# Optimization experiments

Hardware: AMD Instinct MI355X
Metric: run time of the kernel (lower is better)

## Reference

```python
import jax, jax.numpy as jnp
import numpy as np

GAMMA = 0.5
SCALE_BASE = 512.0
LN_EPS = 1e-5


def _xpos(x, downscale=False):
    # x: (B, S, Dh); RetNet XPOS rotary embedding (Jamie-Stirling impl)
    S, Dh = x.shape[1], x.shape[2]
    half = Dh // 2
    base_scale = (jnp.arange(0, Dh, 2, dtype=jnp.float32) + 0.4 * Dh) / (1.4 * Dh)  # (half,)
    power = jnp.arange(S, dtype=jnp.float32)[:, None] / SCALE_BASE                   # (S,1)
    scale = base_scale[None, :] ** power                                             # (S,half)
    inv_freq = 1.0 / (10000.0 ** (jnp.arange(half, dtype=jnp.float32) / half))       # (half,)
    sinusoid = jnp.arange(S, dtype=jnp.float32)[:, None] * inv_freq[None, :]         # (S,half)
    sin, cos = jnp.sin(sinusoid), jnp.cos(sinusoid)
    if downscale:
        scale = 1.0 / scale
    # duplicate_interleave: (S,half) -> (S,Dh) repeating each column twice
    sin_s = jnp.repeat(sin * scale, 2, axis=-1)
    cos_s = jnp.repeat(cos * scale, 2, axis=-1)
    x1, x2 = x[..., ::2], x[..., 1::2]
    rot = jnp.stack((-x2, x1), axis=-1).reshape(x.shape)  # rotate_every_two
    return x * cos_s + rot * sin_s


def _decay_mask(S):
    n = jnp.arange(S)
    diff = (n[:, None] - n[None, :]).astype(jnp.float32)
    return jnp.where(n[:, None] >= n[None, :], GAMMA ** diff, 0.0)  # (S,S)


def setup_inputs() -> dict:
    key = jax.random.key(0)
    ks = jax.random.split(key, 10)
    D, d = 768, 192
    hw, b, s = 196, 8, 32
    x = jax.random.normal(ks[0], (hw, b * s, D), dtype=jnp.float32)
    scale_in = 1.0 / np.sqrt(D)
    scale_d = 1.0 / np.sqrt(d)
    return {
        "x": x,
        "W1": jax.random.normal(ks[1], (D, d), dtype=jnp.float32) * scale_in,
        "b1": jnp.zeros((d,), dtype=jnp.float32),
        "W2": jax.random.normal(ks[2], (d, D), dtype=jnp.float32) * scale_d,
        "b2": jnp.zeros((D,), dtype=jnp.float32),
        "ln_g": jnp.ones((d,), dtype=jnp.float32),
        "ln_b": jnp.zeros((d,), dtype=jnp.float32),
        "WQ": jax.random.normal(ks[3], (d, d), dtype=jnp.float32) * scale_d,
        "WK": jax.random.normal(ks[4], (d, d), dtype=jnp.float32) * scale_d,
        "WV": jax.random.normal(ks[5], (d, d), dtype=jnp.float32) * scale_d,
        "batch_dim": 8,
        "seq_dim": 32,
        "hw": 196,
    }


def reference(x, W1, b1, W2, b2, ln_g, ln_b, WQ, WK, WV, batch_dim, seq_dim, hw):
    D = x.shape[-1]
    # (hw, b*s, D) -> (b*hw, s, D)
    xr = x.reshape(hw, batch_dim, seq_dim, D).transpose(1, 0, 2, 3)
    xr = xr.reshape(batch_dim * hw, seq_dim, D)
    x_down = xr @ W1 + b1  # (B, s, d)
    # LayerNorm
    mu = jnp.mean(x_down, axis=-1, keepdims=True)
    var = jnp.mean((x_down - mu) ** 2, axis=-1, keepdims=True)
    h = (x_down - mu) / jnp.sqrt(var + LN_EPS) * ln_g + ln_b
    # SimpleRetention (parallel form)
    Q = _xpos(h @ WQ, downscale=False)
    K = _xpos(h @ WK, downscale=True)
    V = h @ WV
    Dmask = _decay_mask(seq_dim)  # (s,s)
    att = jnp.einsum("bnd,bmd->bnm", Q, K) * Dmask[None]
    ret = att @ V  # (B, s, d)
    out = xr + (ret @ W2 + b2)
    # (b*hw, s, D) -> (hw, b*s, D)
    out = out.reshape(batch_dim, hw, seq_dim, D).transpose(1, 0, 2, 3)
    return out.reshape(hw, batch_dim * seq_dim, D)
```

## Files before the change

kernel.cpp:

```cpp
#include <hip/hip_runtime.h>

typedef __bf16 bf16x8 __attribute__((ext_vector_type(8)));
typedef __bf16 bf16x4 __attribute__((ext_vector_type(4)));
typedef float floatx4 __attribute__((ext_vector_type(4)));

__device__ __forceinline__ __bf16 f2bf(float f) {
  union { float f; unsigned u; } x; x.f = f;
  unsigned r = (x.u + 0x7FFFu + ((x.u >> 16) & 1u)) >> 16;
  union { unsigned short u; __bf16 b; } o; o.u = (unsigned short)r; return o.b;
}
__device__ __forceinline__ float bf2f(__bf16 b) {
  union { unsigned short u; __bf16 b; } i; i.b = b;
  union { unsigned u; float f; } y; y.u = ((unsigned)i.u) << 16; return y.f;
}

#define MFMA16(a, b, c) __builtin_amdgcn_mfma_f32_16x16x32_bf16(a, b, c, 0, 0, 0)

__global__ __launch_bounds__(256) void prep_weights(
    const float* __restrict__ W1, const float* __restrict__ WQ,
    const float* __restrict__ WK, const float* __restrict__ WV,
    const float* __restrict__ W2,
    __bf16* __restrict__ w1f, __bf16* __restrict__ wqf,
    __bf16* __restrict__ wkf, __bf16* __restrict__ wvf,
    __bf16* __restrict__ w2f) {
  int i = blockIdx.x * 256 + threadIdx.x;
  if (i < 147456) {
    int e = i & 7, lane = (i >> 3) & 63, rest = i >> 9;
    int kk32 = rest % 24, nt = rest / 24;
    int n = nt * 16 + (lane & 15), k = kk32 * 32 + (lane >> 4) * 8 + e;
    w1f[i] = f2bf(W1[k * 192 + n]); return;
  }
  i -= 147456;
  if (i < 36864) {
    int e = i & 7, lane = (i >> 3) & 63, rest = i >> 9;
    int kk32 = rest % 6, nt = rest / 6;
    int n = nt * 16 + (lane & 15), k = kk32 * 32 + (lane >> 4) * 8 + e;
    wqf[i] = f2bf(WQ[k * 192 + n]); return;
  }
  i -= 36864;
  if (i < 36864) {
    int e = i & 7, lane = (i >> 3) & 63, rest = i >> 9;
    int kk32 = rest % 6, nt = rest / 6;
    int n = nt * 16 + (lane & 15), k = kk32 * 32 + (lane >> 4) * 8 + e;
    wkf[i] = f2bf(WK[k * 192 + n]); return;
  }
  i -= 36864;
  if (i < 36864) {
    int e = i & 7, lane = (i >> 3) & 63, rest = i >> 9;
    int kk32 = rest % 6, nt = rest / 6;
    int n = nt * 16 + (lane & 15), k = kk32 * 32 + (lane >> 4) * 8 + e;
    wvf[i] = f2bf(WV[k * 192 + n]); return;
  }
  i -= 36864;
  if (i < 147456) {
    int e = i & 7, lane = (i >> 3) & 63, rest = i >> 9;
    int kk32 = rest % 6, nt = rest / 6;
    int n = nt * 16 + (lane & 15), k = kk32 * 32 + (lane >> 4) * 8 + e;
    w2f[i] = f2bf(W2[k * 768 + n]); return;
  }
}

__global__ __launch_bounds__(256) void prep_xf(
    const float* __restrict__ x, __bf16* __restrict__ xf) {
  int j = blockIdx.x * 256 + threadIdx.x;
  int lane = j & 63;
  int rest = j >> 6;
  int kk32 = rest % 24;
  int rest2 = rest / 24;
  size_t row = (size_t)rest2 * 16 + (lane & 15);
  int d = kk32 * 32 + ((lane >> 4) & 3) * 8;
  const float* src = x + row * 768 + d;
  float4 f0 = *(const float4*)(src);
  float4 f1 = *(const float4*)(src + 4);
  bf16x8 a;
  a[0] = f2bf(f0.x); a[1] = f2bf(f0.y); a[2] = f2bf(f0.z); a[3] = f2bf(f0.w);
  a[4] = f2bf(f1.x); a[5] = f2bf(f1.y); a[6] = f2bf(f1.z); a[7] = f2bf(f1.w);
  *(bf16x8*)(xf + (size_t)j * 8) = a;
}

__global__ __launch_bounds__(256) void prep_tables(
    float* __restrict__ cq, float* __restrict__ sq,
    float* __restrict__ ck, float* __restrict__ sk) {
  int i = blockIdx.x * 256 + threadIdx.x;
  if (i >= 32 * 96) return;
  int s = i / 96, f = i % 96;
  float base = (2.f * f + 0.4f * 192.f) / (1.4f * 192.f);
  float scale = powf(base, (float)s / 512.f);
  float invf = powf(10000.f, -(float)f / 96.f);
  float ang = (float)s * invf;
  float sn = sinf(ang), cs = cosf(ang);
  int o = s * 192 + 2 * f;
  cq[o] = cs * scale; cq[o + 1] = cs * scale;
  sq[o] = sn * scale; sq[o + 1] = sn * scale;
  ck[o] = cs / scale; ck[o + 1] = cs / scale;
  sk[o] = sn / scale; sk[o + 1] = sn / scale;
}

#define SW(r, c) ((r) * 192 + ((c) ^ (((r) & 7) << 3)))

template <bool USE_XF>
__global__ __launch_bounds__(256) void retnet_main(
    const float* __restrict__ x, const float* __restrict__ b1,
    const float* __restrict__ b2, const float* __restrict__ ln_g,
    const float* __restrict__ ln_b,
    const __bf16* __restrict__ w1f, const __bf16* __restrict__ wqf,
    const __bf16* __restrict__ wkf, const __bf16* __restrict__ wvf,
    const __bf16* __restrict__ w2f,
    const float* __restrict__ cq, const float* __restrict__ sq,
    const float* __restrict__ ck, const float* __restrict__ sk,
    const __bf16* __restrict__ xf, float* __restrict__ out) {
  __shared__ __align__(16) char smem[51200];
  __bf16* Q = (__bf16*)smem;
  __bf16* Kl = (__bf16*)(smem + 12288);
  __bf16* Vt = (__bf16*)(smem + 24576);
  __bf16* att = (__bf16*)(smem + 36864);
  __bf16* h = (__bf16*)(smem + 38912);

  const int tid = threadIdx.x;
  const int wv = tid >> 6;
  const int lane = tid & 63;
  const int l16 = lane & 15;
  const int quad = lane >> 4;
  const int kof = quad * 8;
  const int p = blockIdx.x;
  const float* xblk = x + (size_t)p * 32 * 768;

  {
    floatx4 acc[2][3] = {};
    if (USE_XF) {
      const __bf16* xfp = xf + (size_t)p * 24576;
#pragma unroll 4
      for (int kk32 = 0; kk32 < 24; ++kk32) {
        bf16x8 a0 = *(const bf16x8*)(xfp + kk32 * 512 + lane * 8);
        bf16x8 a1 = *(const bf16x8*)(xfp + 12288 + kk32 * 512 + lane * 8);
#pragma unroll
        for (int t = 0; t < 3; ++t) {
          bf16x8 bb = *(const bf16x8*)(w1f + (size_t)((wv * 3 + t) * 24 + kk32) * 512 + lane * 8);
          acc[0][t] = MFMA16(a0, bb, acc[0][t]);
          acc[1][t] = MFMA16(a1, bb, acc[1][t]);
        }
      }
    } else {
      const float* arow0 = xblk + l16 * 768;
      const float* arow1 = xblk + (16 + l16) * 768;
#pragma unroll 2
      for (int kk = 0; kk < 768; kk += 32) {
        float4 f0 = *(const float4*)(arow0 + kk + kof);
        float4 f1 = *(const float4*)(arow0 + kk + kof + 4);
        float4 g0 = *(const float4*)(arow1 + kk + kof);
        float4 g1 = *(const float4*)(arow1 + kk + kof + 4);
        bf16x8 a0, a1;
        a0[0] = f2bf(f0.x); a0[1] = f2bf(f0.y); a0[2] = f2bf(f0.z); a0[3] = f2bf(f0.w);
        a0[4] = f2bf(f1.x); a0[5] = f2bf(f1.y); a0[6] = f2bf(f1.z); a0[7] = f2bf(f1.w);
        a1[0] = f2bf(g0.x); a1[1] = f2bf(g0.y); a1[2] = f2bf(g0.z); a1[3] = f2bf(g0.w);
        a1[4] = f2bf(g1.x); a1[5] = f2bf(g1.y); a1[6] = f2bf(g1.z); a1[7] = f2bf(g1.w);
        int kk32 = kk >> 5;
#pragma unroll
        for (int t = 0; t < 3; ++t) {
          bf16x8 bb = *(const bf16x8*)(w1f + (size_t)((wv * 3 + t) * 24 + kk32) * 512 + lane * 8);
          acc[0][t] = MFMA16(a0, bb, acc[0][t]);
          acc[1][t] = MFMA16(a1, bb, acc[1][t]);
        }
      }
    }
#pragma unroll
    for (int m = 0; m < 2; ++m)
#pragma unroll
      for (int t = 0; t < 3; ++t) {
        int col = wv * 48 + t * 16 + l16;
        float bias = b1[col];
#pragma unroll
        for (int r = 0; r < 4; ++r) {
          int row = m * 16 + quad * 4 + r;
          h[SW(row, col)] = f2bf(acc[m][t][r] + bias);
        }
      }
  }
  __syncthreads();

  {
    int r = tid >> 3, g = tid & 7;
    float vals[24]; float s = 0.f, s2 = 0.f;
#pragma unroll
    for (int j = 0; j < 24; ++j) {
      int c = g * 24 + j;
      float v = bf2f(h[SW(r, c)]);
      vals[j] = v; s += v; s2 += v * v;
    }
#pragma unroll
    for (int o = 1; o < 8; o <<= 1) { s += __shfl_xor(s, o); s2 += __shfl_xor(s2, o); }
    float mu = s * (1.f / 192.f);
    float var = s2 * (1.f / 192.f) - mu * mu;
    float rstd = rsqrtf(var + 1e-5f);
#pragma unroll
    for (int j = 0; j < 24; ++j) {
      int c = g * 24 + j;
      h[SW(r, c)] = f2bf((vals[j] - mu) * rstd * ln_g[c] + ln_b[c]);
    }
  }
  __syncthreads();

  auto gemm_h = [&](const __bf16* __restrict__ Wf, floatx4 (&acc)[2][3]) {
#pragma unroll
    for (int kk32 = 0; kk32 < 6; ++kk32) {
      bf16x8 a0 = *(const bf16x8*)(h + SW(l16, kk32 * 32 + kof));
      bf16x8 a1 = *(const bf16x8*)(h + SW(16 + l16, kk32 * 32 + kof));
#pragma unroll
      for (int t = 0; t < 3; ++t) {
        bf16x8 bb = *(const bf16x8*)(Wf + (size_t)((wv * 3 + t) * 6 + kk32) * 512 + lane * 8);
        acc[0][t] = MFMA16(a0, bb, acc[0][t]);
        acc[1][t] = MFMA16(a1, bb, acc[1][t]);
      }
    }
  };
  {
    floatx4 acc[2][3] = {};
    gemm_h(wqf, acc);
#pragma unroll
    for (int m = 0; m < 2; ++m)
#pragma unroll
      for (int t = 0; t < 3; ++t) {
        int col = wv * 48 + t * 16 + l16;
#pragma unroll
        for (int r = 0; r < 4; ++r) {
          int row = m * 16 + quad * 4 + r;
          float v = acc[m][t][r];
          float pr = __shfl_xor(v, 1);
          float o = v * cq[row * 192 + col] + ((lane & 1) ? pr : -pr) * sq[row * 192 + col];
          Q[SW(row, col)] = f2bf(o);
        }
      }
  }
  {
    floatx4 acc[2][3] = {};
    gemm_h(wkf, acc);
#pragma unroll
    for (int m = 0; m < 2; ++m)
#pragma unroll
      for (int t = 0; t < 3; ++t) {
        int col = wv * 48 + t * 16 + l16;
#pragma unroll
        for (int r = 0; r < 4; ++r) {
          int row = m * 16 + quad * 4 + r;
          float v = acc[m][t][r];
          float pr = __shfl_xor(v, 1);
          float o = v * ck[row * 192 + col] + ((lane & 1) ? pr : -pr) * sk[row * 192 + col];
          Kl[SW(row, col)] = f2bf(o);
        }
      }
  }
  {
    floatx4 acc[2][3] = {};
    gemm_h(wvf, acc);
#pragma unroll
    for (int m = 0; m < 2; ++m)
#pragma unroll
      for (int t = 0; t < 3; ++t) {
        int col = wv * 48 + t * 16 + l16;
        bf16x4 pk;
#pragma unroll
        for (int r = 0; r < 4; ++r) pk[r] = f2bf(acc[m][t][r]);
        *(bf16x4*)(Vt + col * 32 + m * 16 + quad * 4) = pk;
      }
  }
  __syncthreads();

  {
    int mt = wv >> 1, nt = wv & 1;
    floatx4 acc = {0.f, 0.f, 0.f, 0.f};
#pragma unroll
    for (int kk = 0; kk < 192; kk += 32) {
      bf16x8 a = *(const bf16x8*)(Q + SW(mt * 16 + l16, kk + kof));
      bf16x8 bb = *(const bf16x8*)(Kl + SW(nt * 16 + l16, kk + kof));
      acc = MFMA16(a, bb, acc);
    }
#pragma unroll
    for (int r = 0; r < 4; ++r) {
      int i = mt * 16 + quad * 4 + r;
      int j = nt * 16 + l16;
      float v = (i >= j) ? acc[r] * exp2f((float)(j - i)) : 0.f;
      att[i * 32 + j] = f2bf(v);
    }
  }
  __syncthreads();

  {
    floatx4 acc[2][3] = {};
    bf16x8 a0 = *(const bf16x8*)(att + l16 * 32 + kof);
    bf16x8 a1 = *(const bf16x8*)(att + (16 + l16) * 32 + kof);
#pragma unroll
    for (int t = 0; t < 3; ++t) {
      bf16x8 bb = *(const bf16x8*)(Vt + (wv * 48 + t * 16 + l16) * 32 + kof);
      acc[0][t] = MFMA16(a0, bb, acc[0][t]);
      acc[1][t] = MFMA16(a1, bb, acc[1][t]);
    }
#pragma unroll
    for (int m = 0; m < 2; ++m)
#pragma unroll
      for (int t = 0; t < 3; ++t) {
        int col = wv * 48 + t * 16 + l16;
#pragma unroll
        for (int r = 0; r < 4; ++r) {
          int row = m * 16 + quad * 4 + r;
          h[SW(row, col)] = f2bf(acc[m][t][r]);
        }
      }
  }
  __syncthreads();

  {
    bf16x8 af[2][6];
#pragma unroll
    for (int k6 = 0; k6 < 6; ++k6) {
      af[0][k6] = *(const bf16x8*)(h + SW(l16, k6 * 32 + kof));
      af[1][k6] = *(const bf16x8*)(h + SW(16 + l16, k6 * 32 + kof));
    }
#pragma unroll
    for (int g = 0; g < 4; ++g) {
      floatx4 acc[2][3] = {};
#pragma unroll
      for (int k6 = 0; k6 < 6; ++k6) {
#pragma unroll
        for (int t = 0; t < 3; ++t) {
          bf16x8 bb = *(const bf16x8*)(w2f + (size_t)((wv * 12 + g * 3 + t) * 6 + k6) * 512 + lane * 8);
          acc[0][t] = MFMA16(af[0][k6], bb, acc[0][t]);
          acc[1][t] = MFMA16(af[1][k6], bb, acc[1][t]);
        }
      }
#pragma unroll
      for (int m = 0; m < 2; ++m)
#pragma unroll
        for (int t = 0; t < 3; ++t) {
          int col = wv * 192 + g * 48 + t * 16 + l16;
          float bias = b2[col];
#pragma unroll
          for (int r = 0; r < 4; ++r) {
            int row = m * 16 + quad * 4 + r;
            size_t gi = (size_t)p * 24576 + row * 768 + col;
            out[gi] = xblk[row * 768 + col] + acc[m][t][r] + bias;
          }
        }
    }
  }
}

extern "C" void kernel_launch(void* const* d_in, const int* in_sizes, int n_in,
                              void* d_out, int out_size, void* d_ws, size_t ws_size,
                              hipStream_t stream) {
  const float* x = (const float*)d_in[0];
  const float* W1 = (const float*)d_in[1];
  const float* b1 = (const float*)d_in[2];
  const float* W2 = (const float*)d_in[3];
  const float* b2 = (const float*)d_in[4];
  const float* lng = (const float*)d_in[5];
  const float* lnb = (const float*)d_in[6];
  const float* WQ = (const float*)d_in[7];
  const float* WK = (const float*)d_in[8];
  const float* WV = (const float*)d_in[9];
  float* out = (float*)d_out;

  char* ws = (char*)d_ws;
  __bf16* w1f = (__bf16*)(ws + 0);
  __bf16* wqf = (__bf16*)(ws + 294912);
  __bf16* wkf = (__bf16*)(ws + 368640);
  __bf16* wvf = (__bf16*)(ws + 442368);
  __bf16* w2f = (__bf16*)(ws + 516096);
  float* cq = (float*)(ws + 811008);
  float* sq = cq + 6144;
  float* ck = sq + 6144;
  float* sk = ck + 6144;
  const size_t xf_off = 909312;
  const size_t xf_bytes = 77070336;
  bool use_xf = (ws_size >= xf_off + xf_bytes);
  __bf16* xfp = (__bf16*)(ws + xf_off);

  hipLaunchKernelGGL(prep_weights, dim3(1584), dim3(256), 0, stream,
                     W1, WQ, WK, WV, W2, w1f, wqf, wkf, wvf, w2f);
  hipLaunchKernelGGL(prep_tables, dim3(12), dim3(256), 0, stream, cq, sq, ck, sk);
  if (use_xf) {
    hipLaunchKernelGGL(prep_xf, dim3(18816), dim3(256), 0, stream, x, xfp);
    hipLaunchKernelGGL((retnet_main<true>), dim3(1568), dim3(256), 0, stream,
                       x, b1, b2, lng, lnb, w1f, wqf, wkf, wvf, w2f,
                       cq, sq, ck, sk, (const __bf16*)xfp, out);
  } else {
    hipLaunchKernelGGL((retnet_main<false>), dim3(1568), dim3(256), 0, stream,
                       x, b1, b2, lng, lnb, w1f, wqf, wkf, wvf, w2f,
                       cq, sq, ck, sk, (const __bf16*)nullptr, out);
  }
}
```

Before: 452.0 us.

## Stage x conversion through LDS and alias main-kernel shared buffers

prep_xf now processes one 32-row block per workgroup. Each workgroup loads x with fully coalesced float4 reads, converts to bf16 into a swizzled LDS tile, then writes out the MFMA fragment layout. This replaces the previous strided gather. The main kernel's shared memory shrinks by aliasing h/Vt and Q/ret, with V held in registers until h is dead. Att/Vt rows are padded to 36 to avoid LDS bank conflicts. Lower LDS use may raise occupancy, but the aliasing adds ordering constraints that depend on the existing barriers.

```diff
diff --git a/kernel.cpp b/kernel.cpp
--- a/kernel.cpp
+++ b/kernel.cpp
@@ -15,6 +15,9 @@
 }
 
 #define MFMA16(a, b, c) __builtin_amdgcn_mfma_f32_16x16x32_bf16(a, b, c, 0, 0, 0)
+
+#define SW(r, c) ((r) * 192 + ((c) ^ (((r) & 7) << 3)))
+#define SWX(r, c) ((r) * 768 + ((c) ^ (((r) & 7) << 3)))
 
 __global__ __launch_bounds__(256) void prep_weights(
     const float* __restrict__ W1, const float* __restrict__ WQ,
@@ -62,20 +65,30 @@
 
 __global__ __launch_bounds__(256) void prep_xf(
     const float* __restrict__ x, __bf16* __restrict__ xf) {
-  int j = blockIdx.x * 256 + threadIdx.x;
-  int lane = j & 63;
-  int rest = j >> 6;
-  int kk32 = rest % 24;
-  int rest2 = rest / 24;
-  size_t row = (size_t)rest2 * 16 + (lane & 15);
-  int d = kk32 * 32 + ((lane >> 4) & 3) * 8;
-  const float* src = x + row * 768 + d;
-  float4 f0 = *(const float4*)(src);
-  float4 f1 = *(const float4*)(src + 4);
-  bf16x8 a;
-  a[0] = f2bf(f0.x); a[1] = f2bf(f0.y); a[2] = f2bf(f0.z); a[3] = f2bf(f0.w);
-  a[4] = f2bf(f1.x); a[5] = f2bf(f1.y); a[6] = f2bf(f1.z); a[7] = f2bf(f1.w);
-  *(bf16x8*)(xf + (size_t)j * 8) = a;
+  __shared__ __align__(16) __bf16 tile[24576];
+  int p = blockIdx.x;
+  int tid = threadIdx.x;
+  const float* xb = x + (size_t)p * 24576;
+#pragma unroll
+  for (int i = 0; i < 24; ++i) {
+    int idx = i * 256 + tid;
+    float4 v = ((const float4*)xb)[idx];
+    int row = idx / 192, c4 = (idx % 192) * 4;
+    bf16x4 b;
+    b[0] = f2bf(v.x); b[1] = f2bf(v.y); b[2] = f2bf(v.z); b[3] = f2bf(v.w);
+    *(bf16x4*)(&tile[SWX(row, c4)]) = b;
+  }
+  __syncthreads();
+  __bf16* dst = xf + (size_t)p * 24576;
+#pragma unroll
+  for (int w = 0; w < 12; ++w) {
+    int j = w * 256 + tid;
+    int lane = j & 63, rest = j >> 6;
+    int kk32 = rest % 24, mt = rest / 24;
+    int row = mt * 16 + (lane & 15);
+    int col = kk32 * 32 + ((lane >> 4) & 3) * 8;
+    *(bf16x8*)(dst + j * 8) = *(const bf16x8*)(&tile[SWX(row, col)]);
+  }
 }
 
 __global__ __launch_bounds__(256) void prep_tables(
@@ -96,8 +109,6 @@
   sk[o] = sn / scale; sk[o + 1] = sn / scale;
 }
 
-#define SW(r, c) ((r) * 192 + ((c) ^ (((r) & 7) << 3)))
-
 template <bool USE_XF>
 __global__ __launch_bounds__(256) void retnet_main(
     const float* __restrict__ x, const float* __restrict__ b1,
@@ -109,12 +120,13 @@
     const float* __restrict__ cq, const float* __restrict__ sq,
     const float* __restrict__ ck, const float* __restrict__ sk,
     const __bf16* __restrict__ xf, float* __restrict__ out) {
-  __shared__ __align__(16) char smem[51200];
-  __bf16* Q = (__bf16*)smem;
-  __bf16* Kl = (__bf16*)(smem + 12288);
-  __bf16* Vt = (__bf16*)(smem + 24576);
-  __bf16* att = (__bf16*)(smem + 36864);
-  __bf16* h = (__bf16*)(smem + 38912);
+  __shared__ __align__(16) char smem[40704];
+  __bf16* h = (__bf16*)smem;
+  __bf16* Vt = (__bf16*)smem;
+  __bf16* Q = (__bf16*)(smem + 13824);
+  __bf16* ret = (__bf16*)(smem + 13824);
+  __bf16* Kl = (__bf16*)(smem + 26112);
+  __bf16* att = (__bf16*)(smem + 38400);
 
   const int tid = threadIdx.x;
   const int wv = tid >> 6;
@@ -122,8 +134,9 @@
   const int l16 = lane & 15;
   const int quad = lane >> 4;
   const int kof = quad * 8;
+  const int wv3 = wv * 3;
   const int p = blockIdx.x;
-  const float* xblk = x + (size_t)p * 32 * 768;
+  const float* xblk = x + (size_t)p * 24576;
 
   {
     floatx4 acc[2][3] = {};
@@ -135,7 +148,7 @@
         bf16x8 a1 = *(const bf16x8*)(xfp + 12288 + kk32 * 512 + lane * 8);
 #pragma unroll
         for (int t = 0; t < 3; ++t) {
-          bf16x8 bb = *(const bf16x8*)(w1f + (size_t)((wv * 3 + t) * 24 + kk32) * 512 + lane * 8);
+          bf16x8 bb = *(const bf16x8*)(w1f + (size_t)((wv3 + t) * 24 + kk32) * 512 + lane * 8);
           acc[0][t] = MFMA16(a0, bb, acc[0][t]);
           acc[1][t] = MFMA16(a1, bb, acc[1][t]);
         }
@@ -157,7 +170,7 @@
         int kk32 = kk >> 5;
 #pragma unroll
         for (int t = 0; t < 3; ++t) {
-          bf16x8 bb = *(const bf16x8*)(w1f + (size_t)((wv * 3 + t) * 24 + kk32) * 512 + lane * 8);
+          bf16x8 bb = *(const bf16x8*)(w1f + (size_t)((wv3 + t) * 24 + kk32) * 512 + lane * 8);
           acc[0][t] = MFMA16(a0, bb, acc[0][t]);
           acc[1][t] = MFMA16(a1, bb, acc[1][t]);
         }
@@ -207,15 +220,16 @@
       bf16x8 a1 = *(const bf16x8*)(h + SW(16 + l16, kk32 * 32 + kof));
 #pragma unroll
       for (int t = 0; t < 3; ++t) {
-        bf16x8 bb = *(const bf16x8*)(Wf + (size_t)((wv * 3 + t) * 6 + kk32) * 512 + lane * 8);
+        bf16x8 bb = *(const bf16x8*)(Wf + (size_t)((wv3 + t) * 6 + kk32) * 512 + lane * 8);
         acc[0][t] = MFMA16(a0, bb, acc[0][t]);
         acc[1][t] = MFMA16(a1, bb, acc[1][t]);
       }
     }
   };
-  {
-    floatx4 acc[2][3] = {};
-    gemm_h(wqf, acc);
+  bf16x4 vv[2][3];
+  {
+    floatx4 aq[2][3] = {};
+    gemm_h(wqf, aq);
 #pragma unroll
     for (int m = 0; m < 2; ++m)
 #pragma unroll
@@ -224,7 +238,7 @@
 #pragma unroll
         for (int r = 0; r < 4; ++r) {
           int row = m * 16 + quad * 4 + r;
-          float v = acc[m][t][r];
+          float v = aq[m][t][r];
           float pr = __shfl_xor(v, 1);
           float o = v * cq[row * 192 + col] + ((lane & 1) ? pr : -pr) * sq[row * 192 + col];
           Q[SW(row, col)] = f2bf(o);
@@ -232,8 +246,8 @@
       }
   }
   {
-    floatx4 acc[2][3] = {};
-    gemm_h(wkf, acc);
+    floatx4 ak[2][3] = {};
+    gemm_h(wkf, ak);
 #pragma unroll
     for (int m = 0; m < 2; ++m)
 #pragma unroll
@@ -242,7 +256,7 @@
 #pragma unroll
         for (int r = 0; r < 4; ++r) {
           int row = m * 16 + quad * 4 + r;
-          float v = acc[m][t][r];
+          float v = ak[m][t][r];
           float pr = __shfl_xor(v, 1);
           float o = v * ck[row * 192 + col] + ((lane & 1) ? pr : -pr) * sk[row * 192 + col];
           Kl[SW(row, col)] = f2bf(o);
@@ -250,49 +264,52 @@
       }
   }
   {
-    floatx4 acc[2][3] = {};
-    gemm_h(wvf, acc);
+    floatx4 av[2][3] = {};
+    gemm_h(wvf, av);
+#pragma unroll
+    for (int m = 0; m < 2; ++m)
+#pragma unroll
+      for (int t = 0; t < 3; ++t)
+#pragma unroll
+        for (int r = 0; r < 4; ++r) vv[m][t][r] = f2bf(av[m][t][r]);
+  }
+  __syncthreads();
+
+  {
 #pragma unroll
     for (int m = 0; m < 2; ++m)
 #pragma unroll
       for (int t = 0; t < 3; ++t) {
         int col = wv * 48 + t * 16 + l16;
-        bf16x4 pk;
-#pragma unroll
-        for (int r = 0; r < 4; ++r) pk[r] = f2bf(acc[m][t][r]);
-        *(bf16x4*)(Vt + col * 32 + m * 16 + quad * 4) = pk;
-      }
-  }
-  __syncthreads();
-
-  {
+        *(bf16x4*)(Vt + col * 36 + m * 16 + quad * 4) = vv[m][t];
+      }
     int mt = wv >> 1, nt = wv & 1;
-    floatx4 acc = {0.f, 0.f, 0.f, 0.f};
+    floatx4 a4 = {0.f, 0.f, 0.f, 0.f};
 #pragma unroll
     for (int kk = 0; kk < 192; kk += 32) {
       bf16x8 a = *(const bf16x8*)(Q + SW(mt * 16 + l16, kk + kof));
       bf16x8 bb = *(const bf16x8*)(Kl + SW(nt * 16 + l16, kk + kof));
-      acc = MFMA16(a, bb, acc);
+      a4 = MFMA16(a, bb, a4);
     }
 #pragma unroll
     for (int r = 0; r < 4; ++r) {
       int i = mt * 16 + quad * 4 + r;
       int j = nt * 16 + l16;
-      float v = (i >= j) ? acc[r] * exp2f((float)(j - i)) : 0.f;
-      att[i * 32 + j] = f2bf(v);
-    }
-  }
-  __syncthreads();
-
-  {
-    floatx4 acc[2][3] = {};
-    bf16x8 a0 = *(const bf16x8*)(att + l16 * 32 + kof);
-    bf16x8 a1 = *(const bf16x8*)(att + (16 + l16) * 32 + kof);
+      float v = (i >= j) ? a4[r] * exp2f((float)(j - i)) : 0.f;
+      att[i * 36 + j] = f2bf(v);
+    }
+  }
+  __syncthreads();
+
+  {
+    floatx4 ar[2][3] = {};
+    bf16x8 a0 = *(const bf16x8*)(att + l16 * 36 + kof);
+    bf16x8 a1 = *(const bf16x8*)(att + (16 + l16) * 36 + kof);
 #pragma unroll
     for (int t = 0; t < 3; ++t) {
-      bf16x8 bb = *(const bf16x8*)(Vt + (wv * 48 + t * 16 + l16) * 32 + kof);
-      acc[0][t] = MFMA16(a0, bb, acc[0][t]);
-      acc[1][t] = MFMA16(a1, bb, acc[1][t]);
+      bf16x8 bb = *(const bf16x8*)(Vt + (wv * 48 + t * 16 + l16) * 36 + kof);
+      ar[0][t] = MFMA16(a0, bb, ar[0][t]);
+      ar[1][t] = MFMA16(a1, bb, ar[1][t]);
     }
 #pragma unroll
     for (int m = 0; m < 2; ++m)
@@ -302,7 +319,7 @@
 #pragma unroll
         for (int r = 0; r < 4; ++r) {
           int row = m * 16 + quad * 4 + r;
-          h[SW(row, col)] = f2bf(acc[m][t][r]);
+          ret[SW(row, col)] = f2bf(ar[m][t][r]);
         }
       }
   }
@@ -312,19 +329,19 @@
     bf16x8 af[2][6];
 #pragma unroll
     for (int k6 = 0; k6 < 6; ++k6) {
-      af[0][k6] = *(const bf16x8*)(h + SW(l16, k6 * 32 + kof));
-      af[1][k6] = *(const bf16x8*)(h + SW(16 + l16, k6 * 32 + kof));
+      af[0][k6] = *(const bf16x8*)(ret + SW(l16, k6 * 32 + kof));
+      af[1][k6] = *(const bf16x8*)(ret + SW(16 + l16, k6 * 32 + kof));
     }
 #pragma unroll
     for (int g = 0; g < 4; ++g) {
-      floatx4 acc[2][3] = {};
+      floatx4 ao[2][3] = {};
 #pragma unroll
       for (int k6 = 0; k6 < 6; ++k6) {
 #pragma unroll
         for (int t = 0; t < 3; ++t) {
           bf16x8 bb = *(const bf16x8*)(w2f + (size_t)((wv * 12 + g * 3 + t) * 6 + k6) * 512 + lane * 8);
-          acc[0][t] = MFMA16(af[0][k6], bb, acc[0][t]);
-          acc[1][t] = MFMA16(af[1][k6], bb, acc[1][t]);
+          ao[0][t] = MFMA16(af[0][k6], bb, ao[0][t]);
+          ao[1][t] = MFMA16(af[1][k6], bb, ao[1][t]);
         }
       }
 #pragma unroll
@@ -337,7 +354,7 @@
           for (int r = 0; r < 4; ++r) {
             int row = m * 16 + quad * 4 + r;
             size_t gi = (size_t)p * 24576 + row * 768 + col;
-            out[gi] = xblk[row * 768 + col] + acc[m][t][r] + bias;
+            out[gi] = xblk[row * 768 + col] + ao[m][t][r] + bias;
           }
         }
     }
@@ -378,7 +395,7 @@
                      W1, WQ, WK, WV, W2, w1f, wqf, wkf, wvf, w2f);
   hipLaunchKernelGGL(prep_tables, dim3(12), dim3(256), 0, stream, cq, sq, ck, sk);
   if (use_xf) {
-    hipLaunchKernelGGL(prep_xf, dim3(18816), dim3(256), 0, stream, x, xfp);
+    hipLaunchKernelGGL(prep_xf, dim3(1568), dim3(256), 0, stream, x, xfp);
     hipLaunchKernelGGL((retnet_main<true>), dim3(1568), dim3(256), 0, stream,
                        x, b1, b2, lng, lnb, w1f, wqf, wkf, wvf, w2f,
                        cq, sq, ck, sk, (const __bf16*)xfp, out);
```

New measurement: 658.9 us. 1.46x slower.
